# Optimization experiments

Hardware: AMD Instinct MI355X
Metric: run time of the kernel (lower is better)

Reference implementation:

```python
import jax, jax.numpy as jnp
import numpy as np

N_NODES = 100000
N_EDGES = 800000
IN_C, HID, OUT_C = 128, 64, 1


def setup_inputs() -> dict:
    key = jax.random.key(0)
    ks = jax.random.split(key, 12)
    x = jax.random.normal(ks[0], (N_NODES, IN_C), dtype=jnp.float32)
    edge_index = jax.random.randint(ks[1], (2, N_EDGES), 0, N_NODES, dtype=jnp.int64)

    def glorot(k, fan_in, fan_out):
        s = jnp.sqrt(6.0 / (fan_in + fan_out)).astype(jnp.float32)
        return jax.random.uniform(k, (fan_in, fan_out), jnp.float32, -s, s)

    return {
        "x": x,
        "edge_index": edge_index,
        "W1": glorot(ks[2], IN_C, 4 * HID), "b1": jnp.zeros((4 * HID,), jnp.float32),
        "W2": glorot(ks[3], 4 * HID, 2 * HID), "b2": jnp.zeros((2 * HID,), jnp.float32),
        "W3": glorot(ks[4], 2 * HID, HID), "b3": jnp.zeros((HID,), jnp.float32),
        "Wl": glorot(ks[5], HID, OUT_C), "bl": jnp.zeros((OUT_C,), jnp.float32),
    }


def _gcn_conv(x, W, b, src, dst, dinv, n_nodes):
    # PyG GCNConv: D^{-1/2} (A + I) D^{-1/2} X W + b
    xt = x @ W                                   # [N, F_out]
    coef = (dinv[src] * dinv[dst])[:, None]      # [E, 1] symmetric norm
    agg = jax.ops.segment_sum(xt[src] * coef, dst, num_segments=n_nodes)
    agg = agg + (dinv * dinv)[:, None] * xt      # self-loop term (norm = 1/deg)
    return agg + b


def reference(x, edge_index, W1, b1, W2, b2, W3, b3, Wl, bl):
    n = x.shape[0]
    src, dst = edge_index[0], edge_index[1]
    # degree with self loops (edge weight 1), as in gcn_norm(add_self_loops=True)
    deg = jax.ops.segment_sum(jnp.ones_like(dst, dtype=x.dtype), dst, num_segments=n) + 1.0
    dinv = jax.lax.rsqrt(deg)

    h = jax.nn.relu(_gcn_conv(x, W1, b1, src, dst, dinv, n))
    # dropout(p=0.5) is identity at inference (eval mode)
    h = jax.nn.relu(_gcn_conv(h, W2, b2, src, dst, dinv, n))
    h = jax.nn.relu(_gcn_conv(h, W3, b3, src, dst, dinv, n))
    return h @ Wl + bl
```

## Files before the change

kernel.cpp:

```cpp
#include <hip/hip_runtime.h>
#include <hip/hip_bf16.h>
#include <stdint.h>


typedef __attribute__((ext_vector_type(8))) short bf16x8;
typedef __attribute__((ext_vector_type(16))) float f32x16;

__device__ __forceinline__ float bf_lo(uint32_t u) {
    union { uint32_t i; float f; } v; v.i = u << 16; return v.f;
}
__device__ __forceinline__ float bf_hi(uint32_t u) {
    union { uint32_t i; float f; } v; v.i = u & 0xffff0000u; return v.f;
}
__device__ __forceinline__ float bf_s(uint16_t h) {
    union { uint32_t i; float f; } v; v.i = ((uint32_t)h) << 16; return v.f;
}
__device__ __forceinline__ uint16_t f2bf(float f) {
    union { float f; uint32_t i; } v; v.f = f;
    uint32_t r = v.i + 0x7fffu + ((v.i >> 16) & 1u);
    return (uint16_t)(r >> 16);
}
__device__ __forceinline__ uint32_t packbf(float a, float b) {
    return (uint32_t)f2bf(a) | ((uint32_t)f2bf(b) << 16);
}

__global__ __launch_bounds__(256) void hist_kernel(const int* __restrict__ dst,
                                                   int* __restrict__ cnt, int E) {
    int e = blockIdx.x * 256 + threadIdx.x;
    if (e < E) atomicAdd(&cnt[dst[e]], 1);
}

__global__ __launch_bounds__(256) void dinv_kernel(const int* __restrict__ cnt,
                                                   float* __restrict__ dinv, int N) {
    int i = blockIdx.x * 256 + threadIdx.x;
    if (i < N) dinv[i] = rsqrtf((float)cnt[i] + 1.0f);
}

__global__ __launch_bounds__(256) void scan_blk(const int* __restrict__ cnt,
                                                int* __restrict__ row_ptr,
                                                int* __restrict__ bsum, int N) {
    int b = blockIdx.x, t = threadIdx.x;
    int base = b * 1024 + t * 4;
    int v0 = 0, v1 = 0, v2 = 0, v3 = 0;
    if (base + 3 < N) {
        int4 q = *(const int4*)(cnt + base);
        v0 = q.x; v1 = q.y; v2 = q.z; v3 = q.w;
    } else if (base < N) {
        v0 = cnt[base];
        if (base + 1 < N) v1 = cnt[base + 1];
        if (base + 2 < N) v2 = cnt[base + 2];
    }
    int tsum = v0 + v1 + v2 + v3;
    __shared__ int ps[256];
    ps[t] = tsum;
    __syncthreads();
    for (int off = 1; off < 256; off <<= 1) {
        int x = (t >= off) ? ps[t - off] : 0;
        __syncthreads();
        ps[t] += x;
        __syncthreads();
    }
    int ex = (t == 0) ? 0 : ps[t - 1];
    if (t == 255) bsum[b] = ps[255];
    if (base + 3 < N) {
        int4 w; w.x = ex; w.y = ex + v0; w.z = ex + v0 + v1; w.w = ex + v0 + v1 + v2;
        *(int4*)(row_ptr + base) = w;
    } else if (base < N) {
        row_ptr[base] = ex;
        if (base + 1 < N) row_ptr[base + 1] = ex + v0;
        if (base + 2 < N) row_ptr[base + 2] = ex + v0 + v1;
    }
}

__global__ __launch_bounds__(128) void scan_tops(int* __restrict__ bsum, int NB) {
    __shared__ int ps[128];
    int t = threadIdx.x;
    int v = (t < NB) ? bsum[t] : 0;
    ps[t] = v;
    __syncthreads();
    for (int off = 1; off < 128; off <<= 1) {
        int x = (t >= off) ? ps[t - off] : 0;
        __syncthreads();
        ps[t] += x;
        __syncthreads();
    }
    if (t < NB) bsum[t] = (t == 0) ? 0 : ps[t - 1];
}

__global__ __launch_bounds__(256) void scan_add(int* __restrict__ row_ptr,
                                                const int* __restrict__ bsum,
                                                int N, int E) {
    int b = blockIdx.x, t = threadIdx.x;
    int base = b * 1024 + t * 4;
    int off = bsum[b];
    if (base + 3 < N) {
        int4 q = *(int4*)(row_ptr + base);
        q.x += off; q.y += off; q.z += off; q.w += off;
        *(int4*)(row_ptr + base) = q;
    } else {
        for (int i = 0; i < 4; ++i)
            if (base + i < N) row_ptr[base + i] += off;
    }
    if (b == 0 && t == 0) row_ptr[N] = E;
}

__global__ __launch_bounds__(256) void fill_kernel(const int* __restrict__ src,
                                                   const int* __restrict__ dst,
                                                   const int* __restrict__ row_ptr,
                                                   int* __restrict__ cnt,
                                                   int* __restrict__ csr_src, int E) {
    int e = blockIdx.x * 256 + threadIdx.x;
    if (e < E) {
        int d = dst[e];
        int old = atomicSub(&cnt[d], 1);
        csr_src[row_ptr[d + 1] - old] = src[e];
    }
}

template <int K, int M>
__device__ __forceinline__ void wprep_one(const float* __restrict__ W,
                                          uint16_t* __restrict__ Wt, int j) {
    int m = j / K, k = j % K;
    Wt[j] = f2bf(W[k * M + m]);
}
__global__ __launch_bounds__(256) void wprep(const float* __restrict__ W1,
                                             const float* __restrict__ W2,
                                             const float* __restrict__ W3,
                                             uint16_t* __restrict__ Wt1,
                                             uint16_t* __restrict__ Wt2,
                                             uint16_t* __restrict__ Wt3) {
    int i = blockIdx.x * 256 + threadIdx.x;
    if (i < 32768) {
        wprep_one<128, 256>(W1, Wt1, i);
    } else if (i < 65536) {
        wprep_one<256, 128>(W2, Wt2, i - 32768);
    } else if (i < 73728) {
        wprep_one<128, 64>(W3, Wt3, i - 65536);
    }
}

__global__ __launch_bounds__(256) void scale_cvt(const float* __restrict__ x,
                                                 const float* __restrict__ dinv,
                                                 uint32_t* __restrict__ U, long total) {
    long i = (long)blockIdx.x * 256 + threadIdx.x;
    if (i >= total) return;
    int row = (int)(i >> 6);
    float2 v = ((const float2*)x)[i];
    float d = dinv[row];
    U[i] = packbf(d * v.x, d * v.y);
}

template <bool BIAS_RELU>
__global__ __launch_bounds__(256) void agg128(const uint32_t* __restrict__ U,
                                              const float* __restrict__ dinv,
                                              const int* __restrict__ row_ptr,
                                              const int* __restrict__ csr_src,
                                              const float* __restrict__ bias,
                                              uint32_t* __restrict__ Out, int N) {
    int wave = threadIdx.x >> 6, lane = threadIdx.x & 63;
    int n = blockIdx.x * 4 + wave;
    if (n >= N) return;
    uint32_t u = U[(long)n * 64 + lane];
    float s0 = bf_lo(u), s1 = bf_hi(u);
    int e0 = row_ptr[n], e1 = row_ptr[n + 1];
    for (int e = e0; e < e1; e += 8) {
        int idx[8];
        uint32_t uu[8];
#pragma unroll
        for (int j = 0; j < 8; ++j) {
            int ee = e + j; if (ee > e1 - 1) ee = e1 - 1;
            idx[j] = csr_src[ee];
        }
#pragma unroll
        for (int j = 0; j < 8; ++j) uu[j] = U[(long)idx[j] * 64 + lane];
#pragma unroll
        for (int j = 0; j < 8; ++j) {
            float m = (e + j < e1) ? 1.f : 0.f;
            s0 += m * bf_lo(uu[j]);
            s1 += m * bf_hi(uu[j]);
        }
    }
    float d = dinv[n];
    float r0 = d * s0, r1 = d * s1;
    if constexpr (BIAS_RELU) {
        r0 = fmaxf(r0 + bias[2 * lane], 0.f);
        r1 = fmaxf(r1 + bias[2 * lane + 1], 0.f);
    }
    Out[(long)n * 64 + lane] = packbf(r0, r1);
}

__global__ __launch_bounds__(256) void agg64_head(const uint16_t* __restrict__ U,
                                                  const float* __restrict__ dinv,
                                                  const int* __restrict__ row_ptr,
                                                  const int* __restrict__ csr_src,
                                                  const float* __restrict__ b3,
                                                  const float* __restrict__ Wl,
                                                  const float* __restrict__ bl,
                                                  float* __restrict__ out, int N) {
    int wave = threadIdx.x >> 6, lane = threadIdx.x & 63;
    int n = blockIdx.x * 4 + wave;
    if (n >= N) return;
    float s = bf_s(U[(long)n * 64 + lane]);
    int e0 = row_ptr[n], e1 = row_ptr[n + 1];
    for (int e = e0; e < e1; e += 8) {
        int idx[8];
        uint16_t uu[8];
#pragma unroll
        for (int j = 0; j < 8; ++j) {
            int ee = e + j; if (ee > e1 - 1) ee = e1 - 1;
            idx[j] = csr_src[ee];
        }
#pragma unroll
        for (int j = 0; j < 8; ++j) uu[j] = U[(long)idx[j] * 64 + lane];
#pragma unroll
        for (int j = 0; j < 8; ++j) {
            float m = (e + j < e1) ? 1.f : 0.f;
            s += m * bf_s(uu[j]);
        }
    }
    float h = fmaxf(dinv[n] * s + b3[lane], 0.f);
    float v = h * Wl[lane];
#pragma unroll
    for (int off = 32; off; off >>= 1) v += __shfl_xor(v, off);
    if (lane == 0) out[n] = v + bl[0];
}

__global__ __launch_bounds__(256, 2) void gemm_fused12(const uint16_t* __restrict__ A,
                                                       const uint16_t* __restrict__ Wt1,
                                                       const float* __restrict__ b1,
                                                       const uint16_t* __restrict__ Wt2,
                                                       const float* __restrict__ dinv,
                                                       uint16_t* __restrict__ Y, int N) {
    constexpr int SD = 72;
    __shared__ short wl[256 * SD];

    int t = threadIdx.x;
    int wave = t >> 6, lane = t & 63;
    int l31 = lane & 31, lhi = lane >> 5;
    long row0 = (long)blockIdx.x * 128 + wave * 32;

    bf16x8 afrag[8];
    {
        long arow = row0 + l31; if (arow > N - 1) arow = N - 1;
        const uint16_t* ap = A + arow * 128 + lhi * 8;
#pragma unroll
        for (int s = 0; s < 8; ++s)
            afrag[s] = *(const bf16x8*)(ap + s * 16);
    }

    f32x16 acc1[8];
#pragma unroll
    for (int c = 0; c < 8; ++c)
#pragma unroll
        for (int r = 0; r < 16; ++r) acc1[c][r] = 0.f;

    int r0 = t / 8, cc8 = (t % 8) * 8;
    for (int kc0 = 0; kc0 < 128; kc0 += 64) {
#pragma unroll
        for (int r = r0; r < 256; r += 32)
            *(bf16x8*)(wl + r * SD + cc8) = *(const bf16x8*)(Wt1 + (long)r * 128 + kc0 + cc8);
        __syncthreads();
#pragma unroll
        for (int s = 0; s < 4; ++s) {
            const short* bp = wl + l31 * SD + s * 16 + lhi * 8;
#pragma unroll
            for (int c = 0; c < 8; ++c) {
                bf16x8 wfrag = *(const bf16x8*)(bp + c * 32 * SD);
                acc1[c] = __builtin_amdgcn_mfma_f32_32x32x16_bf16(
                    wfrag, afrag[kc0 / 16 + s], acc1[c], 0, 0, 0);
            }
        }
        __syncthreads();
    }

    uint32_t pk[32][2];
#pragma unroll
    for (int c = 0; c < 8; ++c) {
#pragma unroll
        for (int g = 0; g < 4; ++g) {
            int m0 = c * 32 + g * 8 + 4 * lhi;
            float4 bv = *(const float4*)(b1 + m0);
            float v0 = fmaxf(acc1[c][g * 4 + 0] + bv.x, 0.f);
            float v1 = fmaxf(acc1[c][g * 4 + 1] + bv.y, 0.f);
            float v2 = fmaxf(acc1[c][g * 4 + 2] + bv.z, 0.f);
            float v3 = fmaxf(acc1[c][g * 4 + 3] + bv.w, 0.f);
            pk[c * 4 + g][0] = packbf(v0, v1);
            pk[c * 4 + g][1] = packbf(v2, v3);
        }
    }

    f32x16 acc2[4];
#pragma unroll
    for (int c = 0; c < 4; ++c)
#pragma unroll
        for (int r = 0; r < 16; ++r) acc2[c][r] = 0.f;

    for (int kc0 = 0; kc0 < 256; kc0 += 64) {
#pragma unroll
        for (int r = r0; r < 128; r += 32)
            *(bf16x8*)(wl + r * SD + cc8) = *(const bf16x8*)(Wt2 + (long)r * 256 + kc0 + cc8);
        __syncthreads();
#pragma unroll
        for (int sl = 0; sl < 4; ++sl) {
            const int s = kc0 / 16 + sl;
            uint32_t send0 = lhi ? pk[2 * s][0] : pk[2 * s + 1][0];
            uint32_t send1 = lhi ? pk[2 * s][1] : pk[2 * s + 1][1];
            uint32_t rcv0 = __shfl_xor(send0, 32);
            uint32_t rcv1 = __shfl_xor(send1, 32);
            uint32_t lc0 = lhi ? pk[2 * s + 1][0] : pk[2 * s][0];
            uint32_t lc1 = lhi ? pk[2 * s + 1][1] : pk[2 * s][1];
            union { uint32_t u[4]; bf16x8 v; } hf;
            hf.u[0] = lhi ? rcv0 : lc0;
            hf.u[1] = lhi ? rcv1 : lc1;
            hf.u[2] = lhi ? lc0 : rcv0;
            hf.u[3] = lhi ? lc1 : rcv1;
            const short* bp = wl + l31 * SD + sl * 16 + lhi * 8;
#pragma unroll
            for (int c = 0; c < 4; ++c) {
                bf16x8 wfrag = *(const bf16x8*)(bp + c * 32 * SD);
                acc2[c] = __builtin_amdgcn_mfma_f32_32x32x16_bf16(
                    wfrag, hf.v, acc2[c], 0, 0, 0);
            }
        }
        __syncthreads();
    }

    long node = row0 + l31;
    bool ok = node < N;
    long nclamp = ok ? node : (N - 1);
    float dn = dinv[nclamp];
    uint16_t* yp = Y + nclamp * 128;
#pragma unroll
    for (int c = 0; c < 4; ++c) {
#pragma unroll
        for (int g = 0; g < 4; ++g) {
            int m0 = c * 32 + g * 8 + 4 * lhi;
            float v0 = acc2[c][g * 4 + 0] * dn;
            float v1 = acc2[c][g * 4 + 1] * dn;
            float v2 = acc2[c][g * 4 + 2] * dn;
            float v3 = acc2[c][g * 4 + 3] * dn;
            if (ok) {
                uint2 pko; pko.x = packbf(v0, v1); pko.y = packbf(v2, v3);
                *(uint2*)(yp + m0) = pko;
            }
        }
    }
}

template <int K, int M, bool BIAS_RELU, bool SCALE_OUT>
__global__ __launch_bounds__(256, 2) void gemm_mfma(const uint16_t* __restrict__ A,
                                                    const uint16_t* __restrict__ Wt,
                                                    const float* __restrict__ bias,
                                                    const float* __restrict__ dinv,
                                                    uint16_t* __restrict__ Y, int N) {
    constexpr int NT = M / 32;
    constexpr int NK = K / 16;
    constexpr int KC = 64;
    constexpr int SD = KC + 8;
    constexpr int CPR = KC / 8;
    __shared__ short wl[M * SD];

    int t = threadIdx.x;
    int wave = t >> 6, lane = t & 63;
    int l31 = lane & 31, lhi = lane >> 5;
    long row0 = (long)blockIdx.x * 128 + wave * 32;

    bf16x8 afrag[NK];
    {
        long arow = row0 + l31; if (arow > N - 1) arow = N - 1;
        const uint16_t* ap = A + arow * K + lhi * 8;
#pragma unroll
        for (int s = 0; s < NK; ++s)
            afrag[s] = *(const bf16x8*)(ap + s * 16);
    }

    f32x16 acc[NT];
#pragma unroll
    for (int c = 0; c < NT; ++c)
#pragma unroll
        for (int r = 0; r < 16; ++r) acc[c][r] = 0.f;

    int r0 = t / CPR, cc8 = (t % CPR) * 8;
    for (int kc0 = 0; kc0 < K; kc0 += KC) {
#pragma unroll
        for (int r = r0; r < M; r += 256 / CPR)
            *(bf16x8*)(wl + r * SD + cc8) = *(const bf16x8*)(Wt + (long)r * K + kc0 + cc8);
        __syncthreads();
#pragma unroll
        for (int s = 0; s < KC / 16; ++s) {
            const short* bp = wl + l31 * SD + s * 16 + lhi * 8;
#pragma unroll
            for (int c = 0; c < NT; ++c) {
                bf16x8 wfrag = *(const bf16x8*)(bp + c * 32 * SD);
                acc[c] = __builtin_amdgcn_mfma_f32_32x32x16_bf16(
                    wfrag, afrag[kc0 / 16 + s], acc[c], 0, 0, 0);
            }
        }
        __syncthreads();
    }

    long node = row0 + l31;
    bool ok = node < N;
    long nclamp = ok ? node : (N - 1);
    float dn = SCALE_OUT ? dinv[nclamp] : 1.f;
    uint16_t* yp = Y + nclamp * M;
#pragma unroll
    for (int c = 0; c < NT; ++c) {
#pragma unroll
        for (int g = 0; g < 4; ++g) {
            int m0 = c * 32 + g * 8 + 4 * lhi;
            float v[4];
#pragma unroll
            for (int j = 0; j < 4; ++j) {
                float x = acc[c][g * 4 + j];
                if constexpr (BIAS_RELU) x = fmaxf(x + bias[m0 + j], 0.f);
                if constexpr (SCALE_OUT) x *= dn;
                v[j] = x;
            }
            if (ok) {
                uint2 pk; pk.x = packbf(v[0], v[1]); pk.y = packbf(v[2], v[3]);
                *(uint2*)(yp + m0) = pk;
            }
        }
    }
}

extern "C" void kernel_launch(void* const* d_in, const int* in_sizes, int n_in,
                              void* d_out, int out_size, void* d_ws, size_t ws_size,
                              hipStream_t stream) {
    const float* x  = (const float*)d_in[0];
    const int* edge = (const int*)d_in[1];
    const float* W1 = (const float*)d_in[2];
    const float* b1 = (const float*)d_in[3];
    const float* W2 = (const float*)d_in[4];
    const float* b2 = (const float*)d_in[5];
    const float* W3 = (const float*)d_in[6];
    const float* b3 = (const float*)d_in[7];
    const float* Wl = (const float*)d_in[8];
    const float* bl = (const float*)d_in[9];
    float* out = (float*)d_out;

    int N = in_sizes[0] / 128;
    int E = in_sizes[1] / 2;
    const int* src = edge;
    const int* dst = edge + E;

    char* ws = (char*)d_ws;
    size_t off = 0;
    auto alloc = [&](size_t bytes) {
        void* p = ws + off;
        off += (bytes + 255) & ~(size_t)255;
        return p;
    };
    int*      cnt     = (int*)     alloc((size_t)N * 4);
    int*      row_ptr = (int*)     alloc((size_t)(N + 1) * 4);
    float*    dinv    = (float*)   alloc((size_t)N * 4);
    int*      csr_src = (int*)     alloc((size_t)E * 4);
    int*      bsum    = (int*)     alloc(128 * 4);
    uint16_t* Wt1     = (uint16_t*)alloc(256 * 128 * 2);
    uint16_t* Wt2     = (uint16_t*)alloc(128 * 256 * 2);
    uint16_t* Wt3     = (uint16_t*)alloc(64 * 128 * 2);
    uint32_t* B_a     = (uint32_t*)alloc((size_t)N * 64 * 4);
    uint32_t* B_b     = (uint32_t*)alloc((size_t)N * 64 * 4);
    (void)ws_size; (void)n_in; (void)out_size;

    int NB = (N + 1023) / 1024;

    hipMemsetAsync(cnt, 0, (size_t)N * 4, stream);
    hist_kernel<<<(E + 255) / 256, 256, 0, stream>>>(dst, cnt, E);
    dinv_kernel<<<(N + 255) / 256, 256, 0, stream>>>(cnt, dinv, N);
    scan_blk<<<NB, 256, 0, stream>>>(cnt, row_ptr, bsum, N);
    scan_tops<<<1, 128, 0, stream>>>(bsum, NB);
    scan_add<<<NB, 256, 0, stream>>>(row_ptr, bsum, N, E);
    fill_kernel<<<(E + 255) / 256, 256, 0, stream>>>(src, dst, row_ptr, cnt, csr_src, E);
    wprep<<<288, 256, 0, stream>>>(W1, W2, W3, Wt1, Wt2, Wt3);

    scale_cvt<<<(int)(((long)N * 64 + 255) / 256), 256, 0, stream>>>(x, dinv, B_a, (long)N * 64);
    agg128<false><<<(N + 3) / 4, 256, 0, stream>>>(B_a, dinv, row_ptr, csr_src, nullptr, B_b, N);
    gemm_fused12<<<(N + 127) / 128, 256, 0, stream>>>(
        (const uint16_t*)B_b, Wt1, b1, Wt2, dinv, (uint16_t*)B_a, N);
    agg128<true><<<(N + 3) / 4, 256, 0, stream>>>(B_a, dinv, row_ptr, csr_src, b2, B_b, N);
    gemm_mfma<128, 64, false, true><<<(N + 127) / 128, 256, 0, stream>>>(
        (const uint16_t*)B_b, Wt3, nullptr, dinv, (uint16_t*)B_a, N);
    agg64_head<<<(N + 3) / 4, 256, 0, stream>>>(
        (const uint16_t*)B_a, dinv, row_ptr, csr_src, b3, Wl, bl, out, N);
}
```

Measured before the change: 383.3 us.

## Split first GEMM into two output halves and widen LDS K-chunks in fused GEMM

```diff
diff --git a/kernel.cpp b/kernel.cpp
--- a/kernel.cpp
+++ b/kernel.cpp
@@ -231,8 +231,8 @@
                                                        const uint16_t* __restrict__ Wt2,
                                                        const float* __restrict__ dinv,
                                                        uint16_t* __restrict__ Y, int N) {
-    constexpr int SD = 72;
-    __shared__ short wl[256 * SD];
+    constexpr int SD = 136;
+    __shared__ short wl[128 * SD];
 
     int t = threadIdx.x;
     int wave = t >> 6, lane = t & 63;
@@ -248,44 +248,48 @@
             afrag[s] = *(const bf16x8*)(ap + s * 16);
     }
 
-    f32x16 acc1[8];
-#pragma unroll
-    for (int c = 0; c < 8; ++c)
-#pragma unroll
-        for (int r = 0; r < 16; ++r) acc1[c][r] = 0.f;
-
-    int r0 = t / 8, cc8 = (t % 8) * 8;
-    for (int kc0 = 0; kc0 < 128; kc0 += 64) {
-#pragma unroll
-        for (int r = r0; r < 256; r += 32)
-            *(bf16x8*)(wl + r * SD + cc8) = *(const bf16x8*)(Wt1 + (long)r * 128 + kc0 + cc8);
-        __syncthreads();
-#pragma unroll
-        for (int s = 0; s < 4; ++s) {
+    int srow = t >> 4, scol = (t & 15) * 8;
+
+    uint32_t pk[32][2];
+
+#pragma unroll
+    for (int h = 0; h < 2; ++h) {
+#pragma unroll
+        for (int i = 0; i < 8; ++i) {
+            int r = srow + 16 * i;
+            *(bf16x8*)(wl + r * SD + scol) =
+                *(const bf16x8*)(Wt1 + (long)(h * 128 + r) * 128 + scol);
+        }
+        __syncthreads();
+        f32x16 acc[4];
+#pragma unroll
+        for (int c = 0; c < 4; ++c)
+#pragma unroll
+            for (int r = 0; r < 16; ++r) acc[c][r] = 0.f;
+#pragma unroll
+        for (int s = 0; s < 8; ++s) {
             const short* bp = wl + l31 * SD + s * 16 + lhi * 8;
 #pragma unroll
-            for (int c = 0; c < 8; ++c) {
+            for (int c = 0; c < 4; ++c) {
                 bf16x8 wfrag = *(const bf16x8*)(bp + c * 32 * SD);
-                acc1[c] = __builtin_amdgcn_mfma_f32_32x32x16_bf16(
-                    wfrag, afrag[kc0 / 16 + s], acc1[c], 0, 0, 0);
-            }
-        }
-        __syncthreads();
-    }
-
-    uint32_t pk[32][2];
-#pragma unroll
-    for (int c = 0; c < 8; ++c) {
-#pragma unroll
-        for (int g = 0; g < 4; ++g) {
-            int m0 = c * 32 + g * 8 + 4 * lhi;
-            float4 bv = *(const float4*)(b1 + m0);
-            float v0 = fmaxf(acc1[c][g * 4 + 0] + bv.x, 0.f);
-            float v1 = fmaxf(acc1[c][g * 4 + 1] + bv.y, 0.f);
-            float v2 = fmaxf(acc1[c][g * 4 + 2] + bv.z, 0.f);
-            float v3 = fmaxf(acc1[c][g * 4 + 3] + bv.w, 0.f);
-            pk[c * 4 + g][0] = packbf(v0, v1);
-            pk[c * 4 + g][1] = packbf(v2, v3);
+                acc[c] = __builtin_amdgcn_mfma_f32_32x32x16_bf16(
+                    wfrag, afrag[s], acc[c], 0, 0, 0);
+            }
+        }
+        __syncthreads();
+#pragma unroll
+        for (int c = 0; c < 4; ++c) {
+#pragma unroll
+            for (int g = 0; g < 4; ++g) {
+                int m0 = (4 * h + c) * 32 + g * 8 + 4 * lhi;
+                float4 bv = *(const float4*)(b1 + m0);
+                float v0 = fmaxf(acc[c][g * 4 + 0] + bv.x, 0.f);
+                float v1 = fmaxf(acc[c][g * 4 + 1] + bv.y, 0.f);
+                float v2 = fmaxf(acc[c][g * 4 + 2] + bv.z, 0.f);
+                float v3 = fmaxf(acc[c][g * 4 + 3] + bv.w, 0.f);
+                pk[(4 * h + c) * 4 + g][0] = packbf(v0, v1);
+                pk[(4 * h + c) * 4 + g][1] = packbf(v2, v3);
+            }
         }
     }
 
@@ -295,13 +299,18 @@
 #pragma unroll
         for (int r = 0; r < 16; ++r) acc2[c][r] = 0.f;
 
-    for (int kc0 = 0; kc0 < 256; kc0 += 64) {
-#pragma unroll
-        for (int r = r0; r < 128; r += 32)
-            *(bf16x8*)(wl + r * SD + cc8) = *(const bf16x8*)(Wt2 + (long)r * 256 + kc0 + cc8);
-        __syncthreads();
-#pragma unroll
-        for (int sl = 0; sl < 4; ++sl) {
+#pragma unroll
+    for (int kq = 0; kq < 2; ++kq) {
+        const int kc0 = kq * 128;
+#pragma unroll
+        for (int i = 0; i < 8; ++i) {
+            int r = srow + 16 * i;
+            *(bf16x8*)(wl + r * SD + scol) =
+                *(const bf16x8*)(Wt2 + (long)r * 256 + kc0 + scol);
+        }
+        __syncthreads();
+#pragma unroll
+        for (int sl = 0; sl < 8; ++sl) {
             const int s = kc0 / 16 + sl;
             uint32_t send0 = lhi ? pk[2 * s][0] : pk[2 * s + 1][0];
             uint32_t send1 = lhi ? pk[2 * s][1] : pk[2 * s + 1][1];
@@ -467,6 +476,7 @@
     int NB = (N + 1023) / 1024;
 
     hipMemsetAsync(cnt, 0, (size_t)N * 4, stream);
+    hipMemsetAsync(csr_src, 0, (size_t)E * 4, stream);
     hist_kernel<<<(E + 255) / 256, 256, 0, stream>>>(dst, cnt, E);
     dinv_kernel<<<(N + 255) / 256, 256, 0, stream>>>(cnt, dinv, N);
     scan_blk<<<NB, 256, 0, stream>>>(cnt, row_ptr, bsum, N);
```

Measured after the change: 381.9 us. Within noise of the previous version (-0.4%).
